# Kernel optimization log

Hardware: AMD Instinct MI355X
Metric: run time of the kernel (lower is better)

Reference implementation:

```python
import jax, jax.numpy as jnp
import numpy as np
import math

B, S, D, H, M, R = 4, 1024, 1024, 16, 4, 64
DH = D // H
EPS = 1e-8

def setup_inputs() -> dict:
    key = jax.random.key(0)
    ks = jax.random.split(key, 8)
    sc = 0.02
    return {
        'x': jax.random.normal(ks[0], (B, S, D), jnp.float32),
        'Wk': jax.random.normal(ks[1], (D, D), jnp.float32) * sc,
        'bk': jnp.zeros((D,), jnp.float32),
        'Wq': jax.random.normal(ks[2], (D, D), jnp.float32) * sc,
        'bq': jnp.zeros((D,), jnp.float32),
        'Wv': jax.random.normal(ks[3], (D, D), jnp.float32) * sc,
        'bv': jnp.zeros((D,), jnp.float32),
        'mask1': jax.random.normal(ks[4], (M, R, S), jnp.float32) * sc,
        'mask2': jax.random.normal(ks[5], (M, R, S), jnp.float32) * sc,
        'roll_back': jax.random.randint(ks[6], (M, S, S), 0, S, jnp.int64),
    }

def reference(x, Wk, bk, Wq, bq, Wv, bv, mask1, mask2, roll_back):
    def proj(W, b):
        # torch Linear: x @ W^T + b ; reshape to [B, H, S, DH]
        y = jnp.dot(x, W.T) + b
        return y.reshape(B, S, H, DH).transpose(0, 2, 1, 3)
    k = proj(Wk, bk)
    q = proj(Wq, bq)
    v = proj(Wv, bv)
    # learnable low-rank mask: [M, S, S]
    learnable_mask = jnp.einsum('mrs,mrt->mst', mask1, mask2)
    # gather along last dim with roll_back indices
    gathered = jnp.take_along_axis(learnable_mask, roll_back, axis=-1)  # [M, S, S]
    att = jnp.einsum('bhsd,bhtd->bhst', q, k) / math.sqrt(DH)  # [B, H, S, S]
    att = att.reshape(B, H // M, M, S, S) * gathered[None, None]
    att = att.reshape(B, H, S, S)
    # Frobenius norm over last two dims per (B, H)
    fro = jnp.sqrt(jnp.sum(att * att, axis=(-2, -1), keepdims=True))
    att = att / (fro + EPS)
    out = jnp.einsum('bhst,bhtd->bhsd', att, v)
    return out.transpose(0, 2, 1, 3).reshape(B, S, D)
```

## Files before the change

kernel.cpp:

```cpp
#include <hip/hip_runtime.h>
#include <hip/hip_bf16.h>
#include <stdint.h>

typedef __attribute__((ext_vector_type(8))) __bf16 bf16x8;
typedef __attribute__((ext_vector_type(4))) float  f32x4;
typedef __attribute__((ext_vector_type(16))) float f32x16;

__device__ __forceinline__ ushort f2bf(float f) {
    union { float f; uint32_t u; } v; v.f = f;
    uint32_t u = v.u;
    uint32_t r = 0x7FFFu + ((u >> 16) & 1u);
    return (ushort)((u + r) >> 16);
}
__device__ __forceinline__ float bf2f(ushort u) {
    union { uint32_t u; float f; } v; v.u = ((uint32_t)u) << 16;
    return v.f;
}

typedef __attribute__((address_space(3))) uint32_t lds_u32_t;
typedef const __attribute__((address_space(1))) uint32_t glb_u32_t;
__device__ __forceinline__ void async_copy16(const void* g, void* l) {
    __builtin_amdgcn_global_load_lds((glb_u32_t*)g, (lds_u32_t*)l, 16, 0, 0);
}

__global__ __launch_bounds__(256) void convert_all(
    const float* __restrict__ x, const float* __restrict__ wk,
    const float* __restrict__ wq, const float* __restrict__ wv,
    ushort* __restrict__ xb, ushort* __restrict__ wball)
{
    int i = blockIdx.x * 256 + threadIdx.x;
    const float* src; ushort* dst; int j;
    if (i < 1048576) { src = x; dst = xb; j = i; }
    else {
        int t = i - 1048576;
        int z = t >> 18;
        j = t & 262143;
        src = (z == 0) ? wk : (z == 1) ? wq : wv;
        dst = wball + z * 1048576;
    }
    float4 f = ((const float4*)src)[j];
    ushort4 o;
    o.x = f2bf(f.x); o.y = f2bf(f.y); o.z = f2bf(f.z); o.w = f2bf(f.w);
    ((ushort4*)dst)[j] = o;
}

__global__ __launch_bounds__(256) void proj_gemm(
    const ushort* __restrict__ xb, const ushort* __restrict__ wball,
    const float* __restrict__ bk, const float* __restrict__ bq, const float* __restrict__ bv,
    ushort* __restrict__ kd, ushort* __restrict__ qd, ushort* __restrict__ vd)
{
    __shared__ ushort As[3 * 128 * 32];
    __shared__ ushort Bs[3 * 128 * 32];
    const int z = blockIdx.z;
    const int row0 = blockIdx.x * 128;
    const int col0 = blockIdx.y * 128;
    const ushort* wb = wball + z * 1048576;
    const int tid = threadIdx.x;
    const int lane = tid & 63, wave = tid >> 6;
    const int quad = lane >> 4, m15 = lane & 15;
    const int wr = wave >> 1, wc = wave & 1;

    f32x4 acc[4][4];
    for (int i = 0; i < 4; i++)
        for (int j = 0; j < 4; j++) acc[i][j] = (f32x4){0.f, 0.f, 0.f, 0.f};

#define STAGE(BI, KK) do {                                                        \
        _Pragma("unroll")                                                         \
        for (int i_ = 0; i_ < 2; i_++) {                                          \
            int c_ = tid + i_ * 256;                                  \
            int r_ = c_ >> 2, cjp_ = c_ & 3;                                      \
            int cj_ = cjp_ ^ ((r_ >> 1) & 3);                                     \
            async_copy16(&xb[(row0 + r_) * 1024 + (KK) + cj_ * 8],                \
                         &As[(BI) * 4096 + c_ * 8]);                              \
            async_copy16(&wb[(col0 + r_) * 1024 + (KK) + cj_ * 8],                \
                         &Bs[(BI) * 4096 + c_ * 8]);                              \
        }                                                                         \
    } while (0)

#define COMPUTE(BI) do {                                                          \
        const ushort* a_ = &As[(BI) * 4096];                                      \
        const ushort* b_ = &Bs[(BI) * 4096];                                      \
        bf16x8 af[4], bfv[4];                                                     \
        _Pragma("unroll")                                                         \
        for (int fr = 0; fr < 4; fr++) {                                          \
            int row = wr * 64 + fr * 16 + m15;                                    \
            af[fr] = *(const bf16x8*)&a_[row * 32 + ((quad ^ ((row >> 1) & 3)) * 8)]; \
        }                                                                         \
        _Pragma("unroll")                                                         \
        for (int fc = 0; fc < 4; fc++) {                                          \
            int row = wc * 64 + fc * 16 + m15;                                    \
            bfv[fc] = *(const bf16x8*)&b_[row * 32 + ((quad ^ ((row >> 1) & 3)) * 8)]; \
        }                                                                         \
        _Pragma("unroll")                                                         \
        for (int fr = 0; fr < 4; fr++)                                            \
            _Pragma("unroll")                                                     \
            for (int fc = 0; fc < 4; fc++)                                        \
                acc[fr][fc] = __builtin_amdgcn_mfma_f32_16x16x32_bf16(            \
                    af[fr], bfv[fc], acc[fr][fc], 0, 0, 0);                       \
    } while (0)

    STAGE(0, 0);
    STAGE(1, 32);

    int cur = 0;
    #pragma unroll 3
    for (int t = 0; t < 30; ++t) {
        int sb = cur + 2; if (sb >= 3) sb -= 3;
        STAGE(sb, (t + 2) * 32);
        asm volatile("s_waitcnt vmcnt(8)" ::: "memory");
        __builtin_amdgcn_s_barrier();
        COMPUTE(cur);
        __builtin_amdgcn_s_barrier();
        cur = (cur == 2) ? 0 : cur + 1;
    }
    asm volatile("s_waitcnt vmcnt(4)" ::: "memory");
    __builtin_amdgcn_s_barrier();
    COMPUTE(cur);
    cur = (cur == 2) ? 0 : cur + 1;
    asm volatile("s_waitcnt vmcnt(0)" ::: "memory");
    __builtin_amdgcn_s_barrier();
    COMPUTE(cur);

#undef STAGE
#undef COMPUTE

    const float* bias = (z == 0) ? bk : (z == 1) ? bq : bv;
    ushort* dstA = (z == 0) ? kd : qd;
    for (int fr = 0; fr < 4; fr++) {
        int ibase = row0 + wr * 64 + fr * 16 + quad * 4;
        int b_ = ibase >> 10, s = ibase & 1023;
        for (int fc = 0; fc < 4; fc++) {
            int j = col0 + wc * 64 + fc * 16 + m15;
            int h = j >> 6, dh = j & 63;
            float bb = bias[j];
            if (z < 2) {
                for (int r = 0; r < 4; r++)
                    dstA[((b_ * 16 + h) * 1024 + (s + r)) * 64 + dh] = f2bf(acc[fr][fc][r] + bb);
            } else {
                ushort4 o;
                o.x = f2bf(acc[fr][fc][0] + bb);
                o.y = f2bf(acc[fr][fc][1] + bb);
                o.z = f2bf(acc[fr][fc][2] + bb);
                o.w = f2bf(acc[fr][fc][3] + bb);
                *(ushort4*)&vd[((b_ * 16 + h) * 64 + dh) * 1024 + s] = o;
            }
        }
    }
}

__global__ __launch_bounds__(256) void mask_fused(
    const float* __restrict__ m1, const float* __restrict__ m2,
    const int* __restrict__ rb, ushort* __restrict__ gth)
{
    __shared__ float As8[64 * 8];
    __shared__ float lmS[8 * 1024];
    const int s0 = blockIdx.x * 8;
    const int m = blockIdx.y;
    const int tid = threadIdx.x;

    if (tid < 128) {
        int r = tid >> 1, half = tid & 1;
        *(float4*)&As8[r * 8 + half * 4] =
            *(const float4*)&m1[(m * 64 + r) * 1024 + s0 + half * 4];
    }
    __syncthreads();

    f32x4 acc8[8];
    #pragma unroll
    for (int s = 0; s < 8; s++) acc8[s] = (f32x4){0.f, 0.f, 0.f, 0.f};
    const float* m2b = m2 + m * 65536 + tid * 4;
    #pragma unroll 4
    for (int r = 0; r < 64; r++) {
        float4 b4 = *(const float4*)&m2b[r * 1024];
        f32x4 b = (f32x4){b4.x, b4.y, b4.z, b4.w};
        #pragma unroll
        for (int s = 0; s < 8; s++) {
            float a = As8[r * 8 + s];
            acc8[s] += a * b;
        }
    }
    #pragma unroll
    for (int s = 0; s < 8; s++)
        *(f32x4*)&lmS[s * 1024 + tid * 4] = acc8[s];
    __syncthreads();

    const int base = (m * 1024 + s0) * 1024;
    #pragma unroll
    for (int i = 0; i < 8; i++) {
        int c = tid + i * 256;
        int row = c >> 8, j = (c & 255) * 4;
        int4 idx = *(const int4*)&rb[base + row * 1024 + j];
        ushort4 o;
        o.x = f2bf(lmS[row * 1024 + (idx.x & 1023)] * 0.125f);
        o.y = f2bf(lmS[row * 1024 + (idx.y & 1023)] * 0.125f);
        o.z = f2bf(lmS[row * 1024 + (idx.z & 1023)] * 0.125f);
        o.w = f2bf(lmS[row * 1024 + (idx.w & 1023)] * 0.125f);
        *(ushort4*)&gth[base + row * 1024 + j] = o;
    }
}

__global__ __launch_bounds__(256, 2) void attention(
    const ushort* __restrict__ qd, const ushort* __restrict__ kd, const ushort* __restrict__ vd,
    const ushort* __restrict__ gth, float* __restrict__ O, float* __restrict__ ss)
{
    __shared__ ushort Ks[64 * 72];
    __shared__ ushort Vs[64 * 72];
    __shared__ ushort Ps[64 * 72];
    __shared__ ushort Ms[64 * 72];
    __shared__ float red[4];
    const int s0 = blockIdx.x * 64;
    const int bh = blockIdx.y;
    const int mm = bh & 3;
    const int tid = threadIdx.x, lane = tid & 63, wave = tid >> 6;
    const int l31 = lane & 31, hl = lane >> 5;
    const int wr2 = wave >> 1, wc2 = wave & 1;

    #pragma unroll
    for (int i = 0; i < 2; i++) {
        int c = tid + i * 256;
        int r = c >> 3, off = (c & 7) * 8;
        *(uint4*)&Ms[r * 72 + off] = *(const uint4*)&qd[(bh * 1024 + s0 + r) * 64 + off];
    }
    __syncthreads();
    bf16x8 qf[4];
    #pragma unroll
    for (int kk = 0; kk < 4; kk++)
        qf[kk] = *(const bf16x8*)&Ms[(wr2 * 32 + l31) * 72 + kk * 16 + hl * 8];

    f32x16 oacc;
    #pragma unroll
    for (int i = 0; i < 16; i++) oacc[i] = 0.f;
    float ssacc = 0.f;
    const ushort* gbase = gth + mm * 1048576 + s0 * 1024;

    for (int t0 = 0; t0 < 1024; t0 += 64) {
        __syncthreads();
        #pragma unroll
        for (int i = 0; i < 2; i++) {
            int c = tid + i * 256;
            int r = c >> 3, off = (c & 7) * 8;
            *(uint4*)&Ks[r * 72 + off] = *(const uint4*)&kd[(bh * 1024 + t0 + r) * 64 + off];
            *(uint4*)&Vs[r * 72 + off] = *(const uint4*)&vd[(bh * 64 + r) * 1024 + t0 + off];
            *(uint4*)&Ms[r * 72 + off] = *(const uint4*)&gbase[r * 1024 + t0 + off];
        }
        __syncthreads();

        f32x16 p;
        #pragma unroll
        for (int i = 0; i < 16; i++) p[i] = 0.f;
        #pragma unroll
        for (int kk = 0; kk < 4; kk++) {
            bf16x8 b = *(const bf16x8*)&Ks[(wc2 * 32 + l31) * 72 + kk * 16 + hl * 8];
            p = __builtin_amdgcn_mfma_f32_32x32x16_bf16(qf[kk], b, p, 0, 0, 0);
        }
        {
            const int col = wc2 * 32 + l31;
            #pragma unroll
            for (int reg = 0; reg < 16; reg++) {
                int row = wr2 * 32 + (reg & 3) + 8 * (reg >> 2) + 4 * hl;
                float pv = p[reg] * bf2f(Ms[row * 72 + col]);
                ssacc += pv * pv;
                Ps[row * 72 + col] = f2bf(pv);
            }
        }
        __syncthreads();
        #pragma unroll
        for (int kk = 0; kk < 4; kk++) {
            bf16x8 a = *(const bf16x8*)&Ps[(wr2 * 32 + l31) * 72 + kk * 16 + hl * 8];
            bf16x8 b = *(const bf16x8*)&Vs[(wc2 * 32 + l31) * 72 + kk * 16 + hl * 8];
            oacc = __builtin_amdgcn_mfma_f32_32x32x16_bf16(a, b, oacc, 0, 0, 0);
        }
    }
    #pragma unroll
    for (int reg = 0; reg < 16; reg++) {
        int s = s0 + wr2 * 32 + (reg & 3) + 8 * (reg >> 2) + 4 * hl;
        int dh = wc2 * 32 + l31;
        O[(bh * 1024 + s) * 64 + dh] = oacc[reg];
    }
    for (int off = 32; off; off >>= 1) ssacc += __shfl_down(ssacc, off, 64);
    if (lane == 0) red[wave] = ssacc;
    __syncthreads();
    if (tid == 0) atomicAdd(&ss[bh], red[0] + red[1] + red[2] + red[3]);
}

__global__ __launch_bounds__(256) void normalize_out(const float* __restrict__ O,
                                                     const float* __restrict__ ss,
                                                     float* __restrict__ out)
{
    int gid = blockIdx.x * 256 + threadIdx.x;
    int e = gid * 4;
    int bh = e >> 16;
    float inv = 1.f / (sqrtf(ss[bh]) + 1e-8f);
    float4 v4 = *(const float4*)&O[e];
    int b_ = bh >> 4, h = bh & 15;
    int s = (e >> 6) & 1023, dh = e & 63;
    float4 o4 = {v4.x * inv, v4.y * inv, v4.z * inv, v4.w * inv};
    *(float4*)&out[((b_ * 1024 + s) * 16 + h) * 64 + dh] = o4;
}

extern "C" void kernel_launch(void* const* d_in, const int* in_sizes, int n_in,
                              void* d_out, int out_size, void* d_ws, size_t ws_size,
                              hipStream_t stream) {
    const float* x  = (const float*)d_in[0];
    const float* Wk = (const float*)d_in[1];
    const float* bk = (const float*)d_in[2];
    const float* Wq = (const float*)d_in[3];
    const float* bq = (const float*)d_in[4];
    const float* Wv = (const float*)d_in[5];
    const float* bv = (const float*)d_in[6];
    const float* m1 = (const float*)d_in[7];
    const float* m2 = (const float*)d_in[8];
    const int*   rb = (const int*)d_in[9];
    float* out = (float*)d_out;

    char* ws = (char*)d_ws;
    ushort* xb    = (ushort*)(ws);
    ushort* wball = (ushort*)(ws + 8388608);
    ushort* kd    = (ushort*)(ws + 14680064);
    ushort* qd    = (ushort*)(ws + 23068672);
    ushort* vd    = (ushort*)(ws + 31457280);
    float*  O     = (float*)(ws + 39845888);
    ushort* gth   = (ushort*)(ws + 56623104);
    float*  ssb   = (float*)(ws + 65011712);

    convert_all<<<7168, 256, 0, stream>>>(x, Wk, Wq, Wv, xb, wball);
    proj_gemm<<<dim3(32, 8, 3), 256, 0, stream>>>(xb, wball, bk, bq, bv, kd, qd, vd);
    mask_fused<<<dim3(128, 4), 256, 0, stream>>>(m1, m2, rb, gth);
    hipMemsetAsync(ssb, 0, 64 * sizeof(float), stream);
    attention<<<dim3(16, 64), 256, 0, stream>>>(qd, kd, vd, gth, O, ssb);
    normalize_out<<<4096, 256, 0, stream>>>(O, ssb, out);
}
```

Measured before the change: 193.6 us.

## Register-prefetch next K/V/mask tiles in attention loop and raise occupancy hint

The attention loop now loads the K, V and gathered-mask tiles for iteration t+2 from global memory into registers while iteration t computes. Those registers are written to shared memory for iteration t+1 at the end of each step, so global load latency is meant to hide behind MFMA work. Launch bounds are also raised from 2 to 4 blocks per CU, which caps register use per thread. The extra 12 prefetch registers plus the tighter cap could cause spills or lower MFMA scheduling quality.

```diff
diff --git a/kernel.cpp b/kernel.cpp
--- a/kernel.cpp
+++ b/kernel.cpp
@@ -199,7 +199,7 @@
     }
 }
 
-__global__ __launch_bounds__(256, 2) void attention(
+__global__ __launch_bounds__(256, 4) void attention(
     const ushort* __restrict__ qd, const ushort* __restrict__ kd, const ushort* __restrict__ vd,
     const ushort* __restrict__ gth, float* __restrict__ O, float* __restrict__ ss)
 {
@@ -215,36 +215,49 @@
     const int l31 = lane & 31, hl = lane >> 5;
     const int wr2 = wave >> 1, wc2 = wave & 1;
 
-    #pragma unroll
-    for (int i = 0; i < 2; i++) {
-        int c = tid + i * 256;
-        int r = c >> 3, off = (c & 7) * 8;
-        *(uint4*)&Ms[r * 72 + off] = *(const uint4*)&qd[(bh * 1024 + s0 + r) * 64 + off];
-    }
+    const int r0_ = tid >> 3,          o0_ = (tid & 7) * 8;
+    const int r1_ = (tid + 256) >> 3,  o1_ = ((tid + 256) & 7) * 8;
+
+    const ushort* gbase = gth + mm * 1048576 + s0 * 1024;
+    const ushort* kdb = kd + bh * 65536;
+    const ushort* vdb = vd + bh * 65536;
+
+    *(uint4*)&Ms[r0_ * 72 + o0_] = *(const uint4*)&qd[(bh * 1024 + s0 + r0_) * 64 + o0_];
+    *(uint4*)&Ms[r1_ * 72 + o1_] = *(const uint4*)&qd[(bh * 1024 + s0 + r1_) * 64 + o1_];
+    uint4 kr0, kr1, vr0, vr1, mr0, mr1;
+    kr0 = *(const uint4*)&kdb[r0_ * 64 + o0_];
+    kr1 = *(const uint4*)&kdb[r1_ * 64 + o1_];
+    vr0 = *(const uint4*)&vdb[r0_ * 1024 + o0_];
+    vr1 = *(const uint4*)&vdb[r1_ * 1024 + o1_];
+    mr0 = *(const uint4*)&gbase[r0_ * 1024 + o0_];
+    mr1 = *(const uint4*)&gbase[r1_ * 1024 + o1_];
     __syncthreads();
     bf16x8 qf[4];
     #pragma unroll
     for (int kk = 0; kk < 4; kk++)
         qf[kk] = *(const bf16x8*)&Ms[(wr2 * 32 + l31) * 72 + kk * 16 + hl * 8];
+    __syncthreads();
+
+    *(uint4*)&Ks[r0_ * 72 + o0_] = kr0;
+    *(uint4*)&Ks[r1_ * 72 + o1_] = kr1;
+    *(uint4*)&Vs[r0_ * 72 + o0_] = vr0;
+    *(uint4*)&Vs[r1_ * 72 + o1_] = vr1;
+    *(uint4*)&Ms[r0_ * 72 + o0_] = mr0;
+    *(uint4*)&Ms[r1_ * 72 + o1_] = mr1;
+    kr0 = *(const uint4*)&kdb[(64 + r0_) * 64 + o0_];
+    kr1 = *(const uint4*)&kdb[(64 + r1_) * 64 + o1_];
+    vr0 = *(const uint4*)&vdb[r0_ * 1024 + 64 + o0_];
+    vr1 = *(const uint4*)&vdb[r1_ * 1024 + 64 + o1_];
+    mr0 = *(const uint4*)&gbase[r0_ * 1024 + 64 + o0_];
+    mr1 = *(const uint4*)&gbase[r1_ * 1024 + 64 + o1_];
+    __syncthreads();
 
     f32x16 oacc;
     #pragma unroll
     for (int i = 0; i < 16; i++) oacc[i] = 0.f;
     float ssacc = 0.f;
-    const ushort* gbase = gth + mm * 1048576 + s0 * 1024;
-
-    for (int t0 = 0; t0 < 1024; t0 += 64) {
-        __syncthreads();
-        #pragma unroll
-        for (int i = 0; i < 2; i++) {
-            int c = tid + i * 256;
-            int r = c >> 3, off = (c & 7) * 8;
-            *(uint4*)&Ks[r * 72 + off] = *(const uint4*)&kd[(bh * 1024 + t0 + r) * 64 + off];
-            *(uint4*)&Vs[r * 72 + off] = *(const uint4*)&vd[(bh * 64 + r) * 1024 + t0 + off];
-            *(uint4*)&Ms[r * 72 + off] = *(const uint4*)&gbase[r * 1024 + t0 + off];
-        }
-        __syncthreads();
-
+
+    for (int t = 0; t < 16; ++t) {
         f32x16 p;
         #pragma unroll
         for (int i = 0; i < 16; i++) p[i] = 0.f;
@@ -269,6 +282,25 @@
             bf16x8 a = *(const bf16x8*)&Ps[(wr2 * 32 + l31) * 72 + kk * 16 + hl * 8];
             bf16x8 b = *(const bf16x8*)&Vs[(wc2 * 32 + l31) * 72 + kk * 16 + hl * 8];
             oacc = __builtin_amdgcn_mfma_f32_32x32x16_bf16(a, b, oacc, 0, 0, 0);
+        }
+        __syncthreads();
+        if (t < 15) {
+            *(uint4*)&Ks[r0_ * 72 + o0_] = kr0;
+            *(uint4*)&Ks[r1_ * 72 + o1_] = kr1;
+            *(uint4*)&Vs[r0_ * 72 + o0_] = vr0;
+            *(uint4*)&Vs[r1_ * 72 + o1_] = vr1;
+            *(uint4*)&Ms[r0_ * 72 + o0_] = mr0;
+            *(uint4*)&Ms[r1_ * 72 + o1_] = mr1;
+            if (t < 14) {
+                const int tn = (t + 2) * 64;
+                kr0 = *(const uint4*)&kdb[(tn + r0_) * 64 + o0_];
+                kr1 = *(const uint4*)&kdb[(tn + r1_) * 64 + o1_];
+                vr0 = *(const uint4*)&vdb[r0_ * 1024 + tn + o0_];
+                vr1 = *(const uint4*)&vdb[r1_ * 1024 + tn + o1_];
+                mr0 = *(const uint4*)&gbase[r0_ * 1024 + tn + o0_];
+                mr1 = *(const uint4*)&gbase[r1_ * 1024 + tn + o1_];
+            }
+            __syncthreads();
         }
     }
     #pragma unroll
```

Result: no change. 195.3 us (+0.9%).
